# Kernel optimization log

Measured on AMD Instinct MI355X. Metric: run time of the kernel, lower is better.

The kernel has to match this reference:

```python
import jax, jax.numpy as jnp
import numpy as np

B, S, UNITS = 32, 4096, 512

def setup_inputs() -> dict:
    key = jax.random.key(0)
    ks = jax.random.split(key, 5)
    scale = 1.0 / np.sqrt(UNITS)
    return {
        "s_prev": jax.random.normal(ks[0], (B, UNITS), dtype=jnp.float32),
        "hidden_states": jax.random.normal(ks[1], (B, S, UNITS), dtype=jnp.float32),
        "Ww": jax.random.normal(ks[2], (UNITS, UNITS), dtype=jnp.float32) * scale,
        "Wb": jnp.zeros((UNITS,), dtype=jnp.float32),
        "Uw": jax.random.normal(ks[3], (UNITS, UNITS), dtype=jnp.float32) * scale,
        "Ub": jnp.zeros((UNITS,), dtype=jnp.float32),
        "Vw": jax.random.normal(ks[4], (UNITS, 1), dtype=jnp.float32) * scale,
        "Vb": jnp.zeros((1,), dtype=jnp.float32),
    }

def reference(s_prev, hidden_states, Ww, Wb, Uw, Ub, Vw, Vb):
    # W(s_prev): [B, 1, U] so it broadcasts over seq axis
    W_s = (s_prev @ Ww + Wb)[:, None, :]
    # U(hidden_states): [B, S, U]
    U_h = jnp.einsum('bsu,uv->bsv', hidden_states, Uw) + Ub
    score = jnp.tanh(W_s + U_h)                      # [B, S, U]
    logits = jnp.einsum('bsu,uo->bso', score, Vw) + Vb  # [B, S, 1]
    weights = jax.nn.softmax(logits, axis=1)         # softmax over seq axis
    context = jnp.sum(weights * hidden_states, axis=1)  # [B, U]
    return (context, weights)
```

## Files before the change

kernel.cpp:

```cpp
#include <hip/hip_runtime.h>
#include <hip/hip_bf16.h>

#define UNITS 512
#define SEQ   4096
#define BATCH 32

typedef __attribute__((ext_vector_type(8))) __bf16 bf16x8;
typedef __attribute__((ext_vector_type(4))) float  f32x4;

__device__ __forceinline__ int swz128(int l) { return l ^ (((l >> 7) & 7) << 4); }

#define MFMA(A, B, C) __builtin_amdgcn_mfma_f32_16x16x32_bf16(A, B, C, 0, 0, 0)
#define GLL(SRC, DST) __builtin_amdgcn_global_load_lds( \
    (const __attribute__((address_space(1))) void*)(SRC), \
    (__attribute__((address_space(3))) void*)(DST), 16, 0, 0)
#define PK8(X, Y) ({ bf16x8 _o; \
    _o[0]=(__bf16)(X).x; _o[1]=(__bf16)(X).y; _o[2]=(__bf16)(X).z; _o[3]=(__bf16)(X).w; \
    _o[4]=(__bf16)(Y).x; _o[5]=(__bf16)(Y).y; _o[6]=(__bf16)(Y).z; _o[7]=(__bf16)(Y).w; _o; })

__global__ void k_bprep(const float* __restrict__ Uw, __bf16* __restrict__ UwTt) {
    const int c  = blockIdx.x;
    const int gx = blockIdx.y;
    const int t  = blockIdx.z;
    const int nl = threadIdx.x;
    const int n  = gx * 256 + nl;
    const int k0 = t * 64 + c * 8;
    bf16x8 o;
#pragma unroll
    for (int j = 0; j < 8; j++)
        o[j] = (__bf16)Uw[(size_t)(k0 + j) * UNITS + n];
    char* dst = (char*)UwTt + (size_t)(t * 2 + gx) * 32768 + swz128(nl * 128 + c * 16);
    *(bf16x8*)dst = o;
}

__global__ void k_wsrow(const float* __restrict__ s_prev, const float* __restrict__ Ww,
                        const float* __restrict__ Wb, const float* __restrict__ Ub,
                        float* __restrict__ ws_Ws) {
    __shared__ float sp[UNITS];
    int b = blockIdx.x, t = threadIdx.x;
    sp[t] = s_prev[b * UNITS + t];
    sp[t + 256] = s_prev[b * UNITS + t + 256];
    __syncthreads();
    float a0 = Wb[t] + Ub[t];
    float a1 = Wb[t + 256] + Ub[t + 256];
#pragma unroll 8
    for (int u = 0; u < UNITS; u++) {
        float s = sp[u];
        a0 += s * Ww[u * UNITS + t];
        a1 += s * Ww[u * UNITS + t + 256];
    }
    ws_Ws[b * UNITS + t] = a0;
    ws_Ws[b * UNITS + t + 256] = a1;
}

#define NT 8

__launch_bounds__(512, 2)
__global__ void k_logits(const float* __restrict__ hidden, const __bf16* __restrict__ UwTt,
                         const float* __restrict__ wsu, const float* __restrict__ Vw,
                         float* __restrict__ lpart) {
    __shared__ __bf16 Ab[2][256 * 64];
    __shared__ __bf16 Bb[2][256 * 64];
    __shared__ float  lred[256][4];

    const int tid  = threadIdx.x;
    const int lane = tid & 63, wv = tid >> 6;
    const int wm = wv >> 2, wn = wv & 3;
    const int l15 = lane & 15, l4 = lane >> 4;

    const int id = blockIdx.x;
    const int gx = (id >> 3) & 1;
    const int y  = ((id >> 4) << 3) | (id & 7);
    const int m0 = y * 256;
    const int b  = m0 >> 12;

    const int xorv  = (l15 & 7) << 4;
    const int koff0 = (l4 * 16) ^ xorv;
    const int koff1 = (64 + l4 * 16) ^ xorv;
    const int aBase = wm * 16384 + l15 * 128;
    const int bBase = wn * 8192  + l15 * 128;

    const int sr = tid >> 1, sh = tid & 1;
    const float* aPtr = hidden + (size_t)(m0 + sr) * UNITS + sh * 32;
    const int wXor = (sr & 7) << 4;
    int wo0 = sr * 128 + (((sh << 6) | 0 ) ^ wXor);
    int wo1 = sr * 128 + (((sh << 6) | 16) ^ wXor);
    int wo2 = sr * 128 + (((sh << 6) | 32) ^ wXor);
    int wo3 = sr * 128 + (((sh << 6) | 48) ^ wXor);

    const char* bglBase = (const char*)UwTt + (size_t)gx * 32768 + wv * 4096 + lane * 16;

    f32x4 acc[8][4];
#pragma unroll
    for (int i = 0; i < 8; i++)
#pragma unroll
        for (int j = 0; j < 4; j++) acc[i][j] = (f32x4){0.f, 0.f, 0.f, 0.f};

    {
        float4 p0 = *(const float4*)(aPtr + 0);
        float4 p1 = *(const float4*)(aPtr + 4);
        float4 p2 = *(const float4*)(aPtr + 8);
        float4 p3 = *(const float4*)(aPtr + 12);
        float4 p4 = *(const float4*)(aPtr + 16);
        float4 p5 = *(const float4*)(aPtr + 20);
        float4 p6 = *(const float4*)(aPtr + 24);
        float4 p7 = *(const float4*)(aPtr + 28);
        GLL(bglBase,        (char*)Bb[0] + wv * 4096);
        GLL(bglBase + 1024, (char*)Bb[0] + wv * 4096 + 1024);
        GLL(bglBase + 2048, (char*)Bb[0] + wv * 4096 + 2048);
        GLL(bglBase + 3072, (char*)Bb[0] + wv * 4096 + 3072);
        *(bf16x8*)((char*)Ab[0] + wo0) = PK8(p0, p1);
        *(bf16x8*)((char*)Ab[0] + wo1) = PK8(p2, p3);
        *(bf16x8*)((char*)Ab[0] + wo2) = PK8(p4, p5);
        *(bf16x8*)((char*)Ab[0] + wo3) = PK8(p6, p7);
        asm volatile("s_waitcnt vmcnt(0) lgkmcnt(0)" ::: "memory");
        __builtin_amdgcn_s_barrier();
    }

#pragma unroll
    for (int kt = 0; kt < NT; ++kt) {
        char* Ac = (char*)Ab[kt & 1];
        char* Bc = (char*)Bb[kt & 1];
        char* An = (char*)Ab[(kt & 1) ^ 1];
        char* Bn = (char*)Bb[(kt & 1) ^ 1];
        const bool st = (kt < NT - 1);
        const float* ap = aPtr + (kt + 1) * 64;
        const char* bs  = bglBase + (size_t)(kt + 1) * 65536;

        bf16x8 bq[4][2];
        bf16x8 af0k0, af0k1, af1k0, af1k1;
        float4 la0, la1, la2, la3, la4, la5, la6, la7;

#pragma unroll
        for (int fj = 0; fj < 4; fj++) {
            bq[fj][0] = *(const bf16x8*)(Bc + bBase + fj * 2048 + koff0);
            bq[fj][1] = *(const bf16x8*)(Bc + bBase + fj * 2048 + koff1);
        }
        af0k0 = *(const bf16x8*)(Ac + aBase + 0 * 2048 + koff0);
        af0k1 = *(const bf16x8*)(Ac + aBase + 0 * 2048 + koff1);
        af1k0 = *(const bf16x8*)(Ac + aBase + 1 * 2048 + koff0);
        af1k1 = *(const bf16x8*)(Ac + aBase + 1 * 2048 + koff1);
        if (st) {
            la0 = *(const float4*)(ap + 0);
            la1 = *(const float4*)(ap + 4);
            la2 = *(const float4*)(ap + 8);
            la3 = *(const float4*)(ap + 12);
            GLL(bs,        Bn + wv * 4096);
            GLL(bs + 1024, Bn + wv * 4096 + 1024);
        }
        asm volatile("s_waitcnt lgkmcnt(0)" ::: "memory");
        __builtin_amdgcn_sched_barrier(0);
        __builtin_amdgcn_s_setprio(1);
#pragma unroll
        for (int fj = 0; fj < 4; fj++) {
            acc[0][fj] = MFMA(af0k0, bq[fj][0], acc[0][fj]);
            acc[0][fj] = MFMA(af0k1, bq[fj][1], acc[0][fj]);
            acc[1][fj] = MFMA(af1k0, bq[fj][0], acc[1][fj]);
            acc[1][fj] = MFMA(af1k1, bq[fj][1], acc[1][fj]);
        }
        __builtin_amdgcn_s_setprio(0);
        __builtin_amdgcn_s_barrier();

        af0k0 = *(const bf16x8*)(Ac + aBase + 2 * 2048 + koff0);
        af0k1 = *(const bf16x8*)(Ac + aBase + 2 * 2048 + koff1);
        af1k0 = *(const bf16x8*)(Ac + aBase + 3 * 2048 + koff0);
        af1k1 = *(const bf16x8*)(Ac + aBase + 3 * 2048 + koff1);
        if (st) {
            la4 = *(const float4*)(ap + 16);
            la5 = *(const float4*)(ap + 20);
            la6 = *(const float4*)(ap + 24);
            la7 = *(const float4*)(ap + 28);
            GLL(bs + 2048, Bn + wv * 4096 + 2048);
            GLL(bs + 3072, Bn + wv * 4096 + 3072);
            *(bf16x8*)(An + wo0) = PK8(la0, la1);
            *(bf16x8*)(An + wo1) = PK8(la2, la3);
        }
        asm volatile("s_waitcnt lgkmcnt(0)" ::: "memory");
        __builtin_amdgcn_sched_barrier(0);
        __builtin_amdgcn_s_setprio(1);
#pragma unroll
        for (int fj = 0; fj < 4; fj++) {
            acc[2][fj] = MFMA(af0k0, bq[fj][0], acc[2][fj]);
            acc[2][fj] = MFMA(af0k1, bq[fj][1], acc[2][fj]);
            acc[3][fj] = MFMA(af1k0, bq[fj][0], acc[3][fj]);
            acc[3][fj] = MFMA(af1k1, bq[fj][1], acc[3][fj]);
        }
        __builtin_amdgcn_s_setprio(0);
        __builtin_amdgcn_s_barrier();

        af0k0 = *(const bf16x8*)(Ac + aBase + 4 * 2048 + koff0);
        af0k1 = *(const bf16x8*)(Ac + aBase + 4 * 2048 + koff1);
        af1k0 = *(const bf16x8*)(Ac + aBase + 5 * 2048 + koff0);
        af1k1 = *(const bf16x8*)(Ac + aBase + 5 * 2048 + koff1);
        if (st) {
            *(bf16x8*)(An + wo2) = PK8(la4, la5);
        }
        asm volatile("s_waitcnt lgkmcnt(0)" ::: "memory");
        __builtin_amdgcn_sched_barrier(0);
        __builtin_amdgcn_s_setprio(1);
#pragma unroll
        for (int fj = 0; fj < 4; fj++) {
            acc[4][fj] = MFMA(af0k0, bq[fj][0], acc[4][fj]);
            acc[4][fj] = MFMA(af0k1, bq[fj][1], acc[4][fj]);
            acc[5][fj] = MFMA(af1k0, bq[fj][0], acc[5][fj]);
            acc[5][fj] = MFMA(af1k1, bq[fj][1], acc[5][fj]);
        }
        __builtin_amdgcn_s_setprio(0);
        __builtin_amdgcn_s_barrier();

        af0k0 = *(const bf16x8*)(Ac + aBase + 6 * 2048 + koff0);
        af0k1 = *(const bf16x8*)(Ac + aBase + 6 * 2048 + koff1);
        af1k0 = *(const bf16x8*)(Ac + aBase + 7 * 2048 + koff0);
        af1k1 = *(const bf16x8*)(Ac + aBase + 7 * 2048 + koff1);
        if (st) {
            *(bf16x8*)(An + wo3) = PK8(la6, la7);
        }
        asm volatile("s_waitcnt lgkmcnt(0)" ::: "memory");
        __builtin_amdgcn_sched_barrier(0);
        __builtin_amdgcn_s_setprio(1);
#pragma unroll
        for (int fj = 0; fj < 4; fj++) {
            acc[6][fj] = MFMA(af0k0, bq[fj][0], acc[6][fj]);
            acc[6][fj] = MFMA(af0k1, bq[fj][1], acc[6][fj]);
            acc[7][fj] = MFMA(af1k0, bq[fj][0], acc[7][fj]);
            acc[7][fj] = MFMA(af1k1, bq[fj][1], acc[7][fj]);
        }
        __builtin_amdgcn_s_setprio(0);
        if (st) asm volatile("s_waitcnt vmcnt(0)" ::: "memory");
        __builtin_amdgcn_s_barrier();
    }

    float wsub[4], vww[4];
#pragma unroll
    for (int fj = 0; fj < 4; fj++) {
        int n = gx * 256 + wn * 64 + fj * 16 + l15;
        wsub[fj] = wsu[b * UNITS + n];
        vww[fj]  = Vw[n];
    }
#pragma unroll
    for (int fi = 0; fi < 8; fi++) {
#pragma unroll
        for (int r = 0; r < 4; r++) {
            float p = 0.f;
#pragma unroll
            for (int fj = 0; fj < 4; fj++) {
                float x = acc[fi][fj][r] + wsub[fj];
                float e = __expf(2.f * x);
                p += vww[fj] * (1.f - 2.f / (e + 1.f));
            }
#pragma unroll
            for (int off = 1; off < 16; off <<= 1) p += __shfl_xor(p, off);
            if (l15 == 0) lred[wm * 128 + fi * 16 + l4 * 4 + r][wn] = p;
        }
    }
    __syncthreads();
    if (tid < 256) {
        float s = lred[tid][0] + lred[tid][1] + lred[tid][2] + lred[tid][3];
        lpart[(size_t)(m0 + tid) * 2 + gx] = s;
    }
}

__global__ void k_softmax(const float* __restrict__ lpart, float* __restrict__ wout) {
    __shared__ float ebuf[SEQ];
    __shared__ float red[8];
    int b = blockIdx.x, t = threadIdx.x;
    int lane = t & 63, wv = t >> 6;
    float m = -1e30f;
#pragma unroll
    for (int i = 0; i < 16; i++) {
        int s = t + i * 256;
        size_t idx = ((size_t)b * SEQ + s) * 2;
        float l = lpart[idx] + lpart[idx + 1];
        ebuf[s] = l;
        m = fmaxf(m, l);
    }
#pragma unroll
    for (int off = 32; off >= 1; off >>= 1) m = fmaxf(m, __shfl_xor(m, off));
    if (lane == 0) red[wv] = m;
    __syncthreads();
    m = fmaxf(fmaxf(red[0], red[1]), fmaxf(red[2], red[3]));
    float zs = 0.f;
#pragma unroll
    for (int i = 0; i < 16; i++) {
        int s = t + i * 256;
        float e = __expf(ebuf[s] - m);
        ebuf[s] = e;
        zs += e;
    }
#pragma unroll
    for (int off = 32; off >= 1; off >>= 1) zs += __shfl_xor(zs, off);
    __syncthreads();
    if (lane == 0) red[wv] = zs;
    __syncthreads();
    float inv = 1.f / (red[0] + red[1] + red[2] + red[3]);
#pragma unroll
    for (int i = 0; i < 16; i++) {
        int s = t + i * 256;
        wout[(size_t)b * SEQ + s] = ebuf[s] * inv;
    }
}

__global__ void k_ctxpart(const float* __restrict__ hidden, const float* __restrict__ wout,
                          float* __restrict__ part) {
    int b = blockIdx.y, c = blockIdx.x, t = threadIdx.x;
    const float* w = wout + (size_t)b * SEQ + c * 128;
    const float* h = hidden + ((size_t)b * SEQ + c * 128) * UNITS;
    float2 acc = make_float2(0.f, 0.f);
#pragma unroll 4
    for (int s = 0; s < 128; s++) {
        float ww = w[s];
        float2 v = ((const float2*)(h + (size_t)s * UNITS))[t];
        acc.x += ww * v.x;
        acc.y += ww * v.y;
    }
    ((float2*)(part + ((size_t)(b * 32 + c)) * UNITS))[t] = acc;
}

__global__ void k_ctxreduce(const float* __restrict__ part, float* __restrict__ ctx) {
    int b = blockIdx.x, t = threadIdx.x;
    float s = 0.f;
#pragma unroll
    for (int c = 0; c < 32; c++) s += part[((size_t)(b * 32 + c)) * UNITS + t];
    ctx[(size_t)b * UNITS + t] = s;
}

extern "C" void kernel_launch(void* const* d_in, const int* in_sizes, int n_in,
                              void* d_out, int out_size, void* d_ws, size_t ws_size,
                              hipStream_t stream) {
    const float* s_prev = (const float*)d_in[0];
    const float* hidden = (const float*)d_in[1];
    const float* Ww     = (const float*)d_in[2];
    const float* Wb     = (const float*)d_in[3];
    const float* Uw     = (const float*)d_in[4];
    const float* Ub     = (const float*)d_in[5];
    const float* Vw     = (const float*)d_in[6];

    float* out  = (float*)d_out;
    float* ctx  = out;
    float* wout = out + BATCH * UNITS;

    float* wsf   = (float*)d_ws;
    float* ws_Ws = wsf;
    float* ws_lp = ws_Ws + BATCH * UNITS;
    float* ws_cp = ws_lp + (size_t)BATCH * SEQ * 2;
    __bf16* UwTt = (__bf16*)(ws_cp + (size_t)BATCH * 32 * UNITS);

    k_bprep<<<dim3(8, 2, 8), dim3(256), 0, stream>>>(Uw, UwTt);
    k_wsrow<<<dim3(32), dim3(256), 0, stream>>>(s_prev, Ww, Wb, Ub, ws_Ws);
    k_logits<<<dim3(1024), dim3(512), 0, stream>>>(hidden, UwTt, ws_Ws, Vw, ws_lp);
    k_softmax<<<dim3(32), dim3(256), 0, stream>>>(ws_lp, wout);
    k_ctxpart<<<dim3(32, 32), dim3(256), 0, stream>>>(hidden, wout, ws_cp);
    k_ctxreduce<<<dim3(32), dim3(512), 0, stream>>>(ws_cp, ctx);
}
```

Baseline: 255.9 us.

## Prefetch hidden-state A tiles two K-steps ahead with deeper register pipeline

Restructures the k_logits main loop so fp32 hidden-state loads are issued two K-tiles ahead and held in registers across iterations. Their LDS stores and the B-tile global-to-LDS copies move after each MFMA block, and partial vmcnt waits replace the full drain. It also drops the 2-waves-per-SIMD occupancy hint in launch bounds and limits unrolling to 2. The aim is to hide global load latency behind MFMA work, at the cost of more live registers and possibly lower occupancy.

```diff
diff --git a/kernel.cpp b/kernel.cpp
--- a/kernel.cpp
+++ b/kernel.cpp
@@ -55,7 +55,7 @@
 
 #define NT 8
 
-__launch_bounds__(512, 2)
+__launch_bounds__(512)
 __global__ void k_logits(const float* __restrict__ hidden, const __bf16* __restrict__ UwTt,
                          const float* __restrict__ wsu, const float* __restrict__ Vw,
                          float* __restrict__ lpart) {
@@ -83,10 +83,10 @@
     const int sr = tid >> 1, sh = tid & 1;
     const float* aPtr = hidden + (size_t)(m0 + sr) * UNITS + sh * 32;
     const int wXor = (sr & 7) << 4;
-    int wo0 = sr * 128 + (((sh << 6) | 0 ) ^ wXor);
-    int wo1 = sr * 128 + (((sh << 6) | 16) ^ wXor);
-    int wo2 = sr * 128 + (((sh << 6) | 32) ^ wXor);
-    int wo3 = sr * 128 + (((sh << 6) | 48) ^ wXor);
+    const int wo0 = sr * 128 + (((sh << 6) | 0 ) ^ wXor);
+    const int wo1 = sr * 128 + (((sh << 6) | 16) ^ wXor);
+    const int wo2 = sr * 128 + (((sh << 6) | 32) ^ wXor);
+    const int wo3 = sr * 128 + (((sh << 6) | 48) ^ wXor);
 
     const char* bglBase = (const char*)UwTt + (size_t)gx * 32768 + wv * 4096 + lane * 16;
 
@@ -96,40 +96,40 @@
 #pragma unroll
         for (int j = 0; j < 4; j++) acc[i][j] = (f32x4){0.f, 0.f, 0.f, 0.f};
 
+    float4 la0, la1, la2, la3, la4, la5, la6, la7;
+
     {
-        float4 p0 = *(const float4*)(aPtr + 0);
-        float4 p1 = *(const float4*)(aPtr + 4);
-        float4 p2 = *(const float4*)(aPtr + 8);
-        float4 p3 = *(const float4*)(aPtr + 12);
-        float4 p4 = *(const float4*)(aPtr + 16);
-        float4 p5 = *(const float4*)(aPtr + 20);
-        float4 p6 = *(const float4*)(aPtr + 24);
-        float4 p7 = *(const float4*)(aPtr + 28);
+        la0 = *(const float4*)(aPtr + 0);  la1 = *(const float4*)(aPtr + 4);
+        la2 = *(const float4*)(aPtr + 8);  la3 = *(const float4*)(aPtr + 12);
+        la4 = *(const float4*)(aPtr + 16); la5 = *(const float4*)(aPtr + 20);
+        la6 = *(const float4*)(aPtr + 24); la7 = *(const float4*)(aPtr + 28);
         GLL(bglBase,        (char*)Bb[0] + wv * 4096);
         GLL(bglBase + 1024, (char*)Bb[0] + wv * 4096 + 1024);
         GLL(bglBase + 2048, (char*)Bb[0] + wv * 4096 + 2048);
         GLL(bglBase + 3072, (char*)Bb[0] + wv * 4096 + 3072);
-        *(bf16x8*)((char*)Ab[0] + wo0) = PK8(p0, p1);
-        *(bf16x8*)((char*)Ab[0] + wo1) = PK8(p2, p3);
-        *(bf16x8*)((char*)Ab[0] + wo2) = PK8(p4, p5);
-        *(bf16x8*)((char*)Ab[0] + wo3) = PK8(p6, p7);
-        asm volatile("s_waitcnt vmcnt(0) lgkmcnt(0)" ::: "memory");
-        __builtin_amdgcn_s_barrier();
-    }
-
-#pragma unroll
+        *(bf16x8*)((char*)Ab[0] + wo0) = PK8(la0, la1);
+        *(bf16x8*)((char*)Ab[0] + wo1) = PK8(la2, la3);
+        *(bf16x8*)((char*)Ab[0] + wo2) = PK8(la4, la5);
+        *(bf16x8*)((char*)Ab[0] + wo3) = PK8(la6, la7);
+        la0 = *(const float4*)(aPtr + 64);  la1 = *(const float4*)(aPtr + 68);
+        la2 = *(const float4*)(aPtr + 72);  la3 = *(const float4*)(aPtr + 76);
+        la4 = *(const float4*)(aPtr + 80);  la5 = *(const float4*)(aPtr + 84);
+        la6 = *(const float4*)(aPtr + 88);  la7 = *(const float4*)(aPtr + 92);
+        asm volatile("s_waitcnt vmcnt(8) lgkmcnt(0)" ::: "memory");
+        __builtin_amdgcn_s_barrier();
+    }
+
+#pragma unroll 2
     for (int kt = 0; kt < NT; ++kt) {
         char* Ac = (char*)Ab[kt & 1];
         char* Bc = (char*)Bb[kt & 1];
         char* An = (char*)Ab[(kt & 1) ^ 1];
         char* Bn = (char*)Bb[(kt & 1) ^ 1];
-        const bool st = (kt < NT - 1);
-        const float* ap = aPtr + (kt + 1) * 64;
+        const float* ap = aPtr + (kt + 2) * 64;
         const char* bs  = bglBase + (size_t)(kt + 1) * 65536;
 
         bf16x8 bq[4][2];
         bf16x8 af0k0, af0k1, af1k0, af1k1;
-        float4 la0, la1, la2, la3, la4, la5, la6, la7;
 
 #pragma unroll
         for (int fj = 0; fj < 4; fj++) {
@@ -140,14 +140,6 @@
         af0k1 = *(const bf16x8*)(Ac + aBase + 0 * 2048 + koff1);
         af1k0 = *(const bf16x8*)(Ac + aBase + 1 * 2048 + koff0);
         af1k1 = *(const bf16x8*)(Ac + aBase + 1 * 2048 + koff1);
-        if (st) {
-            la0 = *(const float4*)(ap + 0);
-            la1 = *(const float4*)(ap + 4);
-            la2 = *(const float4*)(ap + 8);
-            la3 = *(const float4*)(ap + 12);
-            GLL(bs,        Bn + wv * 4096);
-            GLL(bs + 1024, Bn + wv * 4096 + 1024);
-        }
         asm volatile("s_waitcnt lgkmcnt(0)" ::: "memory");
         __builtin_amdgcn_sched_barrier(0);
         __builtin_amdgcn_s_setprio(1);
@@ -159,22 +151,20 @@
             acc[1][fj] = MFMA(af1k1, bq[fj][1], acc[1][fj]);
         }
         __builtin_amdgcn_s_setprio(0);
+        __builtin_amdgcn_sched_barrier(0);
+        if (kt < NT - 1) {
+            *(bf16x8*)(An + wo0) = PK8(la0, la1);
+            GLL(bs,        Bn + wv * 4096);
+            GLL(bs + 1024, Bn + wv * 4096 + 1024);
+            GLL(bs + 2048, Bn + wv * 4096 + 2048);
+            GLL(bs + 3072, Bn + wv * 4096 + 3072);
+        }
         __builtin_amdgcn_s_barrier();
 
         af0k0 = *(const bf16x8*)(Ac + aBase + 2 * 2048 + koff0);
         af0k1 = *(const bf16x8*)(Ac + aBase + 2 * 2048 + koff1);
         af1k0 = *(const bf16x8*)(Ac + aBase + 3 * 2048 + koff0);
         af1k1 = *(const bf16x8*)(Ac + aBase + 3 * 2048 + koff1);
-        if (st) {
-            la4 = *(const float4*)(ap + 16);
-            la5 = *(const float4*)(ap + 20);
-            la6 = *(const float4*)(ap + 24);
-            la7 = *(const float4*)(ap + 28);
-            GLL(bs + 2048, Bn + wv * 4096 + 2048);
-            GLL(bs + 3072, Bn + wv * 4096 + 3072);
-            *(bf16x8*)(An + wo0) = PK8(la0, la1);
-            *(bf16x8*)(An + wo1) = PK8(la2, la3);
-        }
         asm volatile("s_waitcnt lgkmcnt(0)" ::: "memory");
         __builtin_amdgcn_sched_barrier(0);
         __builtin_amdgcn_s_setprio(1);
@@ -186,15 +176,14 @@
             acc[3][fj] = MFMA(af1k1, bq[fj][1], acc[3][fj]);
         }
         __builtin_amdgcn_s_setprio(0);
+        __builtin_amdgcn_sched_barrier(0);
+        if (kt < NT - 1) *(bf16x8*)(An + wo1) = PK8(la2, la3);
         __builtin_amdgcn_s_barrier();
 
         af0k0 = *(const bf16x8*)(Ac + aBase + 4 * 2048 + koff0);
         af0k1 = *(const bf16x8*)(Ac + aBase + 4 * 2048 + koff1);
         af1k0 = *(const bf16x8*)(Ac + aBase + 5 * 2048 + koff0);
         af1k1 = *(const bf16x8*)(Ac + aBase + 5 * 2048 + koff1);
-        if (st) {
-            *(bf16x8*)(An + wo2) = PK8(la4, la5);
-        }
         asm volatile("s_waitcnt lgkmcnt(0)" ::: "memory");
         __builtin_amdgcn_sched_barrier(0);
         __builtin_amdgcn_s_setprio(1);
@@ -206,15 +195,18 @@
             acc[5][fj] = MFMA(af1k1, bq[fj][1], acc[5][fj]);
         }
         __builtin_amdgcn_s_setprio(0);
+        __builtin_amdgcn_sched_barrier(0);
+        if (kt < NT - 1) *(bf16x8*)(An + wo2) = PK8(la4, la5);
+        if (kt < NT - 2) {
+            la0 = *(const float4*)(ap + 0);  la1 = *(const float4*)(ap + 4);
+            la2 = *(const float4*)(ap + 8);  la3 = *(const float4*)(ap + 12);
+        }
         __builtin_amdgcn_s_barrier();
 
         af0k0 = *(const bf16x8*)(Ac + aBase + 6 * 2048 + koff0);
         af0k1 = *(const bf16x8*)(Ac + aBase + 6 * 2048 + koff1);
         af1k0 = *(const bf16x8*)(Ac + aBase + 7 * 2048 + koff0);
         af1k1 = *(const bf16x8*)(Ac + aBase + 7 * 2048 + koff1);
-        if (st) {
-            *(bf16x8*)(An + wo3) = PK8(la6, la7);
-        }
         asm volatile("s_waitcnt lgkmcnt(0)" ::: "memory");
         __builtin_amdgcn_sched_barrier(0);
         __builtin_amdgcn_s_setprio(1);
@@ -226,7 +218,15 @@
             acc[7][fj] = MFMA(af1k1, bq[fj][1], acc[7][fj]);
         }
         __builtin_amdgcn_s_setprio(0);
-        if (st) asm volatile("s_waitcnt vmcnt(0)" ::: "memory");
+        __builtin_amdgcn_sched_barrier(0);
+        if (kt < NT - 1) *(bf16x8*)(An + wo3) = PK8(la6, la7);
+        if (kt < NT - 2) {
+            la4 = *(const float4*)(ap + 16); la5 = *(const float4*)(ap + 20);
+            la6 = *(const float4*)(ap + 24); la7 = *(const float4*)(ap + 28);
+            asm volatile("s_waitcnt vmcnt(8) lgkmcnt(0)" ::: "memory");
+        } else if (kt == NT - 2) {
+            asm volatile("s_waitcnt vmcnt(0) lgkmcnt(0)" ::: "memory");
+        }
         __builtin_amdgcn_s_barrier();
     }
 
```

Result: faster. 238.9 us (-6.6%).
